# Performance work log

Measured on AMD Instinct MI355X. Metric: run time of the kernel, lower is better.

The kernel has to match this reference:

```python
import jax, jax.numpy as jnp
import numpy as np

B, N, C = 4, 1024, 768          # batch, tokens, embed_dim
D, H, HD, FF = 12, 12, 64, 3072  # depth, heads, head_dim, mlp hidden
LN_EPS = 1e-5


def setup_inputs() -> dict:
    key = jax.random.key(0)
    ks = jax.random.split(key, 12)
    w = lambda i, shape: jax.random.normal(ks[i], shape, jnp.float32) * 0.02
    return {
        "x": jax.random.normal(ks[0], (B, N, C), jnp.float32),
        "pos_x": jax.random.normal(ks[1], (B, N, C), jnp.float32),
        # stacked per-layer params (leading dim D)
        "qkv_w": w(2, (D, 3 * C, C)), "qkv_b": w(3, (D, 3 * C)),
        "proj_w": w(4, (D, C, C)),    "proj_b": w(5, (D, C)),
        "fc1_w": w(6, (D, FF, C)),    "fc1_b": w(7, (D, FF)),
        "fc2_w": w(8, (D, C, FF)),    "fc2_b": w(9, (D, C)),
        "ln1_g": jnp.ones((D, C), jnp.float32), "ln1_b": jnp.zeros((D, C), jnp.float32),
        "ln2_g": jnp.ones((D, C), jnp.float32), "ln2_b": jnp.zeros((D, C), jnp.float32),
        "normf_g": jnp.ones((C,), jnp.float32), "normf_b": jnp.zeros((C,), jnp.float32),
    }


def _ln(x, g, b):
    mu = jnp.mean(x, axis=-1, keepdims=True)
    var = jnp.mean((x - mu) ** 2, axis=-1, keepdims=True)
    return (x - mu) * jax.lax.rsqrt(var + LN_EPS) * g + b


def reference(x, pos_x, qkv_w, qkv_b, proj_w, proj_b, fc1_w, fc1_b, fc2_w, fc2_b,
              ln1_g, ln1_b, ln2_g, ln2_b, normf_g, normf_b):
    scale = 1.0 / jnp.sqrt(jnp.float32(HD))
    x = x + pos_x  # pos added once (add_pos_at_every_layer=False)

    def block(xc, p):
        qw, qb, pw, pb, f1w, f1b, f2w, f2b, g1, b1, g2, b2 = p
        h = _ln(xc, g1, b1)
        qkv = jnp.einsum('bnc,oc->bno', h, qw) + qb            # [B,N,3C]
        qkv = qkv.reshape(B, N, 3, H, HD).transpose(2, 0, 3, 1, 4)
        q, k, v = qkv[0], qkv[1], qkv[2]                       # [B,H,N,HD]
        attn = jax.nn.softmax(jnp.einsum('bhnd,bhmd->bhnm', q, k) * scale, axis=-1)
        o = jnp.einsum('bhnm,bhmd->bhnd', attn, v)
        o = o.transpose(0, 2, 1, 3).reshape(B, N, C)
        xc = xc + (jnp.einsum('bnc,oc->bno', o, pw) + pb)      # residual + proj
        h2 = _ln(xc, g2, b2)
        hid = jax.nn.gelu(jnp.einsum('bnc,fc->bnf', h2, f1w) + f1b, approximate=False)
        ffn = jnp.einsum('bnf,of->bno', hid, f2w) + f2b
        xc = xc + ffn
        return xc, None

    xs = (qkv_w, qkv_b, proj_w, proj_b, fc1_w, fc1_b, fc2_w, fc2_b,
          ln1_g, ln1_b, ln2_g, ln2_b)
    x, _ = jax.lax.scan(block, x, xs)
    return _ln(x, normf_g, normf_b)  # postnorm
```

## Files before the change

kernel.cpp:

```cpp
#include <hip/hip_runtime.h>
#include <hip/hip_bf16.h>
#include <math.h>

typedef __bf16 bf16;
typedef __bf16 bf16x8 __attribute__((ext_vector_type(8)));
typedef __bf16 bf16x4 __attribute__((ext_vector_type(4)));
typedef float  f32x4  __attribute__((ext_vector_type(4)));

#define B_  4
#define N_  1024
#define C_  768
#define H_  12
#define HD_ 64
#define FF_ 3072
#define T_  (B_*N_)
#define D_  12

__device__ __forceinline__ void gld_lds16(const void* g, void* l) {
    __builtin_amdgcn_global_load_lds(
        (const __attribute__((address_space(1))) void*)g,
        (__attribute__((address_space(3))) void*)l, 16, 0, 0);
}

__device__ __forceinline__ float gelu_f(float v) {
    const float ax = fabsf(v) * 0.70710678118f;
    const float t  = __frcp_rn(1.0f + 0.3275911f * ax);
    float p = 1.061405429f;
    p = p * t - 1.453152027f;
    p = p * t + 1.421413741f;
    p = p * t - 0.284496736f;
    p = p * t + 0.254829592f;
    const float e = p * t * __expf(-ax * ax);
    const float erfv = (v >= 0.f) ? (1.0f - e) : (e - 1.0f);
    return 0.5f * v * (1.0f + erfv);
}

template<typename WT, int MODE>
__global__ __launch_bounds__(256) void gemm_bt(
    const bf16* __restrict__ A, const WT* __restrict__ Bt,
    const float* __restrict__ bias, bf16* __restrict__ out,
    float* __restrict__ resid, int M, int N, int Kfull, int Ks)
{
    constexpr int NB = (sizeof(WT) == 2) ? 2 : 1;
    __shared__ __align__(16) bf16 lA[NB][128*64];
    __shared__ __align__(16) WT   lB[NB][128*64];
    const int tid  = threadIdx.x;
    const int lane = tid & 63, wave = tid >> 6;
    const int lo = lane & 15, hi = lane >> 4;
    const int wm = wave & 1, wn = wave >> 1;

    const int nblk = gridDim.x;
    const int id2  = (blockIdx.x & 7) * (nblk >> 3) + (blockIdx.x >> 3);
    const int gx = M >> 7, gy = N >> 7;
    const int bx  = id2 % gx;
    const int byz = id2 / gx;
    const int by  = byz % gy;
    const int bz  = byz / gy;
    const int row0 = bx * 128, col0 = by * 128;
    const int k0base = bz * Ks;
    const int nt = Ks >> 6;

    f32x4 acc[4][4];
#pragma unroll
    for (int i = 0; i < 4; i++)
#pragma unroll
        for (int j = 0; j < 4; j++) acc[i][j] = (f32x4){0.f, 0.f, 0.f, 0.f};

    auto stageA = [&](int t, int buf) {
#pragma unroll
        for (int r = 0; r < 4; ++r) {
            const int cb    = r * 256 + wave * 64;
            const int chunk = cb + lane;
            const int rw = chunk >> 3, kc = chunk & 7;
            const int kcs = kc ^ (rw & 7);
            gld_lds16(A + (size_t)(row0 + rw) * Kfull + k0base + t * 64 + kcs * 8,
                      lA[buf] + cb * 8);
        }
    };
    auto stageB = [&](int t, int buf) {
        if constexpr (sizeof(WT) == 2) {
#pragma unroll
            for (int r = 0; r < 4; ++r) {
                const int cb    = r * 256 + wave * 64;
                const int chunk = cb + lane;
                const int rw = chunk >> 3, kc = chunk & 7;
                const int kcs = kc ^ (rw & 7);
                gld_lds16(Bt + (size_t)(col0 + rw) * Kfull + k0base + t * 64 + kcs * 8,
                          (bf16*)lB[buf] + cb * 8);
            }
        } else {
#pragma unroll
            for (int r = 0; r < 8; ++r) {
                const int cb    = r * 256 + wave * 64;
                const int chunk = cb + lane;
                const int rw = chunk >> 4, kc = chunk & 15;
                const int kcs = kc ^ ((rw & 7) << 1);
                gld_lds16(Bt + (size_t)(col0 + rw) * Kfull + k0base + t * 64 + kcs * 4,
                          (float*)lB[buf] + cb * 4);
            }
        }
    };
    auto compute = [&](int buf) {
#pragma unroll 1
        for (int s = 0; s < 2; ++s) {
            bf16x8 af[4], bfr[4];
#pragma unroll
            for (int i = 0; i < 4; i++) {
                const int rowA = wm * 64 + i * 16 + lo;
                const int ca = (s * 4 + hi) ^ (lo & 7);
                af[i] = *(const bf16x8*)(lA[buf] + rowA * 64 + ca * 8);
            }
#pragma unroll
            for (int i = 0; i < 4; i++) {
                const int rowB = wn * 64 + i * 16 + lo;
                if constexpr (sizeof(WT) == 2) {
                    const int cc = (s * 4 + hi) ^ (lo & 7);
                    bfr[i] = *(const bf16x8*)((const bf16*)lB[buf] + rowB * 64 + cc * 8);
                } else {
                    const float* base = (const float*)lB[buf] + rowB * 64;
                    const int c0 = (s * 8 + hi * 2) ^ ((lo & 7) << 1);
                    const f32x4 u0 = *(const f32x4*)(base + c0 * 4);
                    const f32x4 u1 = *(const f32x4*)(base + (c0 + 1) * 4);
                    bf16x8 f;
#pragma unroll
                    for (int e = 0; e < 4; e++) { f[e] = (bf16)u0[e]; f[4+e] = (bf16)u1[e]; }
                    bfr[i] = f;
                }
            }
#pragma unroll
            for (int mi = 0; mi < 4; mi++)
#pragma unroll
                for (int ni = 0; ni < 4; ni++)
                    acc[mi][ni] = __builtin_amdgcn_mfma_f32_16x16x32_bf16(
                        af[mi], bfr[ni], acc[mi][ni], 0, 0, 0);
        }
    };

    if constexpr (NB == 2) {
        stageA(0, 0); stageB(0, 0);
        __syncthreads();
        int cur = 0;
        for (int t = 0; t < nt; ++t) {
            if (t + 1 < nt) { stageA(t + 1, cur ^ 1); stageB(t + 1, cur ^ 1); }
            compute(cur);
            __syncthreads();
            cur ^= 1;
        }
    } else {
        for (int t = 0; t < nt; ++t) {
            stageA(t, 0); stageB(t, 0);
            __syncthreads();
            compute(0);
            __syncthreads();
        }
    }

    const float bscale = (bz == 0) ? 1.0f : 0.0f;
#pragma unroll
    for (int mi = 0; mi < 4; mi++) {
#pragma unroll
        for (int ni = 0; ni < 4; ni++) {
            const int gcol = col0 + wn * 64 + ni * 16 + lo;
            const float bv = bias[gcol] * bscale;
#pragma unroll
            for (int r = 0; r < 4; r++) {
                const int grow = row0 + wm * 64 + mi * 16 + hi * 4 + r;
                float v = acc[mi][ni][r] + bv;
                if (MODE == 1) v = gelu_f(v);
                if (MODE == 2) {
                    atomicAdd(&resid[(size_t)grow * N + gcol], v);
                } else {
                    out[(size_t)grow * N + gcol] = (bf16)v;
                }
            }
        }
    }
}

__global__ __launch_bounds__(256) void cvt_k(
    const float* __restrict__ src, bf16* __restrict__ dst)
{
    const int i = (blockIdx.x * 256 + threadIdx.x) * 8;
    const f32x4 a = *(const f32x4*)(src + i);
    const f32x4 b = *(const f32x4*)(src + i + 4);
    bf16x8 o;
#pragma unroll
    for (int e = 0; e < 4; e++) { o[e] = (bf16)a[e]; o[4 + e] = (bf16)b[e]; }
    *(bf16x8*)(dst + i) = o;
}

template<typename OutT>
__global__ __launch_bounds__(256) void ln_k(
    const float* __restrict__ x, const float* __restrict__ g,
    const float* __restrict__ b, OutT* __restrict__ out)
{
    const int wave = threadIdx.x >> 6, lane = threadIdx.x & 63;
    const int t = blockIdx.x * 4 + wave;
    const float* row = x + (size_t)t * C_;
    f32x4 v[3];
    float s = 0.f, ss = 0.f;
#pragma unroll
    for (int j = 0; j < 3; j++) {
        v[j] = *(const f32x4*)(row + (j * 64 + lane) * 4);
#pragma unroll
        for (int e = 0; e < 4; e++) { s += v[j][e]; ss += v[j][e] * v[j][e]; }
    }
#pragma unroll
    for (int off = 32; off > 0; off >>= 1) {
        s  += __shfl_xor(s, off);
        ss += __shfl_xor(ss, off);
    }
    const float mu  = s * (1.f / 768.f);
    const float var = ss * (1.f / 768.f) - mu * mu;
    const float rs  = rsqrtf(var + 1e-5f);
    OutT* orow = out + (size_t)t * C_;
#pragma unroll
    for (int j = 0; j < 3; j++) {
        const f32x4 gv = *(const f32x4*)(g + (j * 64 + lane) * 4);
        const f32x4 bv = *(const f32x4*)(b + (j * 64 + lane) * 4);
#pragma unroll
        for (int e = 0; e < 4; e++)
            orow[(j * 64 + lane) * 4 + e] = (OutT)((v[j][e] - mu) * rs * gv[e] + bv[e]);
    }
}

__global__ __launch_bounds__(256) void addpos_k(
    const float* __restrict__ x, const float* __restrict__ p, float* __restrict__ o)
{
    const int i = (blockIdx.x * 256 + threadIdx.x) * 4;
    const f32x4 xv = *(const f32x4*)(x + i);
    const f32x4 pv = *(const f32x4*)(p + i);
    f32x4 ov;
#pragma unroll
    for (int e = 0; e < 4; e++) ov[e] = xv[e] + pv[e];
    *(f32x4*)(o + i) = ov;
}

#define SKD_ 72
#define SVK_ 136
#define SPK_ 136
__global__ __launch_bounds__(256) void attn_k(
    const bf16* __restrict__ qkv, bf16* __restrict__ out)
{
    const int id2 = (blockIdx.x & 7) * 96 + (blockIdx.x >> 3);
    const int qt = id2 & 15;
    const int bh = id2 >> 4;
    const int b = bh / H_, h = bh % H_;
    const int lane = threadIdx.x & 63, wave = threadIdx.x >> 6;
    const int lo = lane & 15, hi = lane >> 4;

    __shared__ __align__(16) bf16 lK[128 * SKD_];
    __shared__ __align__(16) bf16 lV[64 * SVK_];
    __shared__ __align__(16) bf16 lP[4][16 * SPK_];

    const size_t tokbase = (size_t)b * N_;

    const bf16* qptr = qkv + (tokbase + qt * 64 + wave * 16 + lo) * (3 * C_) + h * HD_;
    bf16x8 qf0 = *(const bf16x8*)(qptr + hi * 8);
    bf16x8 qf1 = *(const bf16x8*)(qptr + 32 + hi * 8);
#pragma unroll
    for (int e = 0; e < 8; e++) {
        qf0[e] = (bf16)((float)qf0[e] * 0.125f);
        qf1[e] = (bf16)((float)qf1[e] * 0.125f);
    }

    float m_r[4], l_r[4];
    f32x4 oacc[4];
#pragma unroll
    for (int r = 0; r < 4; r++) { m_r[r] = -1e30f; l_r[r] = 0.f; }
#pragma unroll
    for (int di = 0; di < 4; di++) oacc[di] = (f32x4){0.f, 0.f, 0.f, 0.f};

    for (int kt = 0; kt < 8; ++kt) {
        const int kb0 = kt * 128;
#pragma unroll
        for (int r = 0; r < 4; ++r) {
            const int chunk = r * 256 + threadIdx.x;
            const int key = chunk >> 3, dc = chunk & 7;
            const bf16* kp = qkv + (tokbase + kb0 + key) * (3 * C_) + C_ + h * HD_ + dc * 8;
            *(bf16x8*)(lK + key * SKD_ + dc * 8) = *(const bf16x8*)kp;
        }
#pragma unroll
        for (int r = 0; r < 4; ++r) {
            const int chunk = r * 256 + threadIdx.x;
            const int d = chunk & 63, kg = chunk >> 6;
            const bf16* vp = qkv + (tokbase + kb0 + kg * 8) * (3 * C_)
                           + 2 * C_ + h * HD_ + d;
            bf16x8 tv;
#pragma unroll
            for (int i = 0; i < 8; i++) tv[i] = vp[(size_t)i * (3 * C_)];
            *(bf16x8*)(lV + d * SVK_ + kg * 8) = tv;
        }
        __syncthreads();

        f32x4 sacc[8];
#pragma unroll
        for (int kb = 0; kb < 8; kb++) {
            const bf16x8 b0 = *(const bf16x8*)(lK + (kb * 16 + lo) * SKD_ + hi * 8);
            const bf16x8 b1 = *(const bf16x8*)(lK + (kb * 16 + lo) * SKD_ + 32 + hi * 8);
            f32x4 a = (f32x4){0.f, 0.f, 0.f, 0.f};
            a = __builtin_amdgcn_mfma_f32_16x16x32_bf16(qf0, b0, a, 0, 0, 0);
            a = __builtin_amdgcn_mfma_f32_16x16x32_bf16(qf1, b1, a, 0, 0, 0);
            sacc[kb] = a;
        }

        float pm[4], mn[4], ts[4];
#pragma unroll
        for (int r = 0; r < 4; r++) {
            float a0 = fmaxf(fmaxf(sacc[0][r], sacc[1][r]),
                             fmaxf(sacc[2][r], sacc[3][r]));
            float a1 = fmaxf(fmaxf(sacc[4][r], sacc[5][r]),
                             fmaxf(sacc[6][r], sacc[7][r]));
            pm[r] = fmaxf(a0, a1);
            ts[r] = 0.f;
        }
        const int okd = (pm[0] <= m_r[0] + 8.f) && (pm[1] <= m_r[1] + 8.f)
                     && (pm[2] <= m_r[2] + 8.f) && (pm[3] <= m_r[3] + 8.f);
        const bool defer = __all(okd);
        if (defer) {
#pragma unroll
            for (int r = 0; r < 4; r++) mn[r] = m_r[r];
        } else {
#pragma unroll
            for (int r = 0; r < 4; r++) {
                float tm = pm[r];
#pragma unroll
                for (int off = 1; off < 16; off <<= 1)
                    tm = fmaxf(tm, __shfl_xor(tm, off));
                mn[r] = fmaxf(m_r[r], tm);
            }
        }
#pragma unroll
        for (int kb = 0; kb < 8; kb++)
#pragma unroll
            for (int r = 0; r < 4; r++) {
                const float p = __expf(sacc[kb][r] - mn[r]);
                lP[wave][(hi * 4 + r) * SPK_ + kb * 16 + lo] = (bf16)p;
                ts[r] += p;
            }
#pragma unroll
        for (int r = 0; r < 4; r++)
#pragma unroll
            for (int off = 1; off < 16; off <<= 1)
                ts[r] += __shfl_xor(ts[r], off);
        if (defer) {
#pragma unroll
            for (int r = 0; r < 4; r++) l_r[r] += ts[r];
        } else {
            float alpha[4];
#pragma unroll
            for (int r = 0; r < 4; r++) {
                alpha[r] = __expf(m_r[r] - mn[r]);
                l_r[r] = l_r[r] * alpha[r] + ts[r];
                m_r[r] = mn[r];
            }
#pragma unroll
            for (int di = 0; di < 4; di++)
#pragma unroll
                for (int r = 0; r < 4; r++) oacc[di][r] *= alpha[r];
        }

        bf16x8 pa[4];
#pragma unroll
        for (int s = 0; s < 4; s++)
            pa[s] = *(const bf16x8*)(&lP[wave][lo * SPK_ + s * 32 + hi * 8]);
#pragma unroll
        for (int di = 0; di < 4; di++) {
#pragma unroll
            for (int s = 0; s < 4; s++) {
                const bf16x8 v = *(const bf16x8*)(lV + (di * 16 + lo) * SVK_ + s * 32 + hi * 8);
                oacc[di] = __builtin_amdgcn_mfma_f32_16x16x32_bf16(pa[s], v, oacc[di], 0, 0, 0);
            }
        }
        __syncthreads();
    }

    float il[4];
#pragma unroll
    for (int r = 0; r < 4; r++) il[r] = 1.0f / l_r[r];
#pragma unroll
    for (int di = 0; di < 4; di++)
#pragma unroll
        for (int r = 0; r < 4; r++) {
            const size_t tok = tokbase + qt * 64 + wave * 16 + hi * 4 + r;
            out[tok * C_ + h * HD_ + di * 16 + lo] = (bf16)(oacc[di][r] * il[r]);
        }
}

extern "C" void kernel_launch(void* const* d_in, const int* in_sizes, int n_in,
                              void* d_out, int out_size, void* d_ws, size_t ws_size,
                              hipStream_t stream)
{
    const float* x      = (const float*)d_in[0];
    const float* pos_x  = (const float*)d_in[1];
    const float* qkv_w  = (const float*)d_in[2];
    const float* qkv_b  = (const float*)d_in[3];
    const float* proj_w = (const float*)d_in[4];
    const float* proj_b = (const float*)d_in[5];
    const float* fc1_w  = (const float*)d_in[6];
    const float* fc1_b  = (const float*)d_in[7];
    const float* fc2_w  = (const float*)d_in[8];
    const float* fc2_b  = (const float*)d_in[9];
    const float* ln1_g  = (const float*)d_in[10];
    const float* ln1_b  = (const float*)d_in[11];
    const float* ln2_g  = (const float*)d_in[12];
    const float* ln2_b  = (const float*)d_in[13];
    const float* nf_g   = (const float*)d_in[14];
    const float* nf_b   = (const float*)d_in[15];

    char* ws = (char*)d_ws;
    float* xres  = (float*)(ws);
    bf16* hbuf   = (bf16*)(ws + 12582912);
    bf16* qkvbuf = (bf16*)(ws + 18874368);
    bf16* attno  = (bf16*)(ws + 37748736);
    bf16* hid    = (bf16*)(ws + 44040192);
    bf16* wq     = (bf16*)(ws + 69206016);
    bf16* wp     = (bf16*)(ws + 111673344);
    bf16* w1     = (bf16*)(ws + 125829120);
    bf16* w2     = (bf16*)(ws + 182452224);
    const bool usebf16 = ws_size >= (size_t)239075328;

    addpos_k<<<T_ * C_ / 4 / 256, 256, 0, stream>>>(x, pos_x, xres);

    if (usebf16) {
        cvt_k<<<D_ * 3 * C_ * C_ / 2048, 256, 0, stream>>>(qkv_w, wq);
        cvt_k<<<D_ * C_ * C_ / 2048, 256, 0, stream>>>(proj_w, wp);
        cvt_k<<<D_ * FF_ * C_ / 2048, 256, 0, stream>>>(fc1_w, w1);
        cvt_k<<<D_ * C_ * FF_ / 2048, 256, 0, stream>>>(fc2_w, w2);
    }

    const int g_qkv  = (T_/128) * ((3*C_)/128);
    const int g_proj = (T_/128) * (C_/128) * 2;
    const int g_fc1  = (T_/128) * (FF_/128);
    const int g_fc2  = (T_/128) * (C_/128) * 2;

    for (int L = 0; L < D_; ++L) {
        ln_k<bf16><<<T_ / 4, 256, 0, stream>>>(xres, ln1_g + L * C_, ln1_b + L * C_, hbuf);
        if (usebf16) {
            gemm_bt<bf16,0><<<g_qkv, 256, 0, stream>>>(
                hbuf, wq + (size_t)L * 3 * C_ * C_, qkv_b + (size_t)L * 3 * C_,
                qkvbuf, nullptr, T_, 3 * C_, C_, C_);
        } else {
            gemm_bt<float,0><<<g_qkv, 256, 0, stream>>>(
                hbuf, qkv_w + (size_t)L * 3 * C_ * C_, qkv_b + (size_t)L * 3 * C_,
                qkvbuf, nullptr, T_, 3 * C_, C_, C_);
        }
        attn_k<<<N_ / 64 * B_ * H_, 256, 0, stream>>>(qkvbuf, attno);
        if (usebf16) {
            gemm_bt<bf16,2><<<g_proj, 256, 0, stream>>>(
                attno, wp + (size_t)L * C_ * C_, proj_b + (size_t)L * C_,
                nullptr, xres, T_, C_, C_, C_ / 2);
        } else {
            gemm_bt<float,2><<<g_proj, 256, 0, stream>>>(
                attno, proj_w + (size_t)L * C_ * C_, proj_b + (size_t)L * C_,
                nullptr, xres, T_, C_, C_, C_ / 2);
        }
        ln_k<bf16><<<T_ / 4, 256, 0, stream>>>(xres, ln2_g + L * C_, ln2_b + L * C_, hbuf);
        if (usebf16) {
            gemm_bt<bf16,1><<<g_fc1, 256, 0, stream>>>(
                hbuf, w1 + (size_t)L * FF_ * C_, fc1_b + (size_t)L * FF_,
                hid, nullptr, T_, FF_, C_, C_);
            gemm_bt<bf16,2><<<g_fc2, 256, 0, stream>>>(
                hid, w2 + (size_t)L * C_ * FF_, fc2_b + (size_t)L * C_,
                nullptr, xres, T_, C_, FF_, FF_ / 2);
        } else {
            gemm_bt<float,1><<<g_fc1, 256, 0, stream>>>(
                hbuf, fc1_w + (size_t)L * FF_ * C_, fc1_b + (size_t)L * FF_,
                hid, nullptr, T_, FF_, C_, C_);
            gemm_bt<float,2><<<g_fc2, 256, 0, stream>>>(
                hid, fc2_w + (size_t)L * C_ * FF_, fc2_b + (size_t)L * C_,
                nullptr, xres, T_, C_, FF_, FF_ / 2);
        }
    }
    ln_k<float><<<T_ / 4, 256, 0, stream>>>(xres, nf_g, nf_b, (float*)d_out);
}
```

Measured before the change: 2.878 ms.

## Triple-buffer bf16 GEMM with BK=32 and explicit vmcnt waits

Changes the bf16-weight GEMM path from double-buffered BK=64 tiles to triple-buffered BK=32 tiles. It prefetches two stages ahead and uses explicit s_waitcnt vmcnt counts with raw barriers instead of __syncthreads, so global loads overlap compute more. The LDS footprint per block shrinks, which may raise occupancy, but each barrier now covers only half as much MFMA work. The fp32-weight path is inlined and keeps the same behaviour.

```diff
diff --git a/kernel.cpp b/kernel.cpp
--- a/kernel.cpp
+++ b/kernel.cpp
@@ -21,6 +21,9 @@
         (const __attribute__((address_space(1))) void*)g,
         (__attribute__((address_space(3))) void*)l, 16, 0, 0);
 }
+
+#define WAITV(N) asm volatile("s_waitcnt vmcnt(" #N ")" ::: "memory")
+#define WAITL0() asm volatile("s_waitcnt lgkmcnt(0)" ::: "memory")
 
 __device__ __forceinline__ float gelu_f(float v) {
     const float ax = fabsf(v) * 0.70710678118f;
@@ -41,9 +44,11 @@
     const float* __restrict__ bias, bf16* __restrict__ out,
     float* __restrict__ resid, int M, int N, int Kfull, int Ks)
 {
-    constexpr int NB = (sizeof(WT) == 2) ? 2 : 1;
-    __shared__ __align__(16) bf16 lA[NB][128*64];
-    __shared__ __align__(16) WT   lB[NB][128*64];
+    constexpr bool BF  = (sizeof(WT) == 2);
+    constexpr int  BK  = BF ? 32 : 64;
+    constexpr int  NBF = BF ? 3 : 1;
+    __shared__ __align__(16) bf16 lA[NBF][128*BK];
+    __shared__ __align__(16) WT   lB[NBF][128*BK];
     const int tid  = threadIdx.x;
     const int lane = tid & 63, wave = tid >> 6;
     const int lo = lane & 15, hi = lane >> 4;
@@ -58,7 +63,7 @@
     const int bz  = byz / gy;
     const int row0 = bx * 128, col0 = by * 128;
     const int k0base = bz * Ks;
-    const int nt = Ks >> 6;
+    const int nt = Ks / BK;
 
     f32x4 acc[4][4];
 #pragma unroll
@@ -66,29 +71,84 @@
 #pragma unroll
         for (int j = 0; j < 4; j++) acc[i][j] = (f32x4){0.f, 0.f, 0.f, 0.f};
 
-    auto stageA = [&](int t, int buf) {
-#pragma unroll
-        for (int r = 0; r < 4; ++r) {
-            const int cb    = r * 256 + wave * 64;
-            const int chunk = cb + lane;
-            const int rw = chunk >> 3, kc = chunk & 7;
-            const int kcs = kc ^ (rw & 7);
-            gld_lds16(A + (size_t)(row0 + rw) * Kfull + k0base + t * 64 + kcs * 8,
-                      lA[buf] + cb * 8);
-        }
-    };
-    auto stageB = [&](int t, int buf) {
-        if constexpr (sizeof(WT) == 2) {
+    if constexpr (BF) {
+        auto stageA = [&](int t, int buf) {
+#pragma unroll
+            for (int r = 0; r < 2; ++r) {
+                const int cb    = r * 256 + wave * 64;
+                const int chunk = cb + lane;
+                const int rw = chunk >> 2, kc = chunk & 3;
+                const int kcs = kc ^ (rw & 3);
+                gld_lds16(A + (size_t)(row0 + rw) * Kfull + k0base + t * 32 + kcs * 8,
+                          lA[buf] + cb * 8);
+            }
+        };
+        auto stageB = [&](int t, int buf) {
+#pragma unroll
+            for (int r = 0; r < 2; ++r) {
+                const int cb    = r * 256 + wave * 64;
+                const int chunk = cb + lane;
+                const int rw = chunk >> 2, kc = chunk & 3;
+                const int kcs = kc ^ (rw & 3);
+                gld_lds16(Bt + (size_t)(col0 + rw) * Kfull + k0base + t * 32 + kcs * 8,
+                          (bf16*)lB[buf] + cb * 8);
+            }
+        };
+        auto compute = [&](int buf) {
+            bf16x8 af[4], bfr[4];
+#pragma unroll
+            for (int i = 0; i < 4; i++) {
+                const int rowA = wm * 64 + i * 16 + lo;
+                const int ca = hi ^ (lo & 3);
+                af[i] = *(const bf16x8*)(lA[buf] + rowA * 32 + ca * 8);
+            }
+#pragma unroll
+            for (int i = 0; i < 4; i++) {
+                const int rowB = wn * 64 + i * 16 + lo;
+                const int cc = hi ^ (lo & 3);
+                bfr[i] = *(const bf16x8*)((const bf16*)lB[buf] + rowB * 32 + cc * 8);
+            }
+#pragma unroll
+            for (int mi = 0; mi < 4; mi++)
+#pragma unroll
+                for (int ni = 0; ni < 4; ni++)
+                    acc[mi][ni] = __builtin_amdgcn_mfma_f32_16x16x32_bf16(
+                        af[mi], bfr[ni], acc[mi][ni], 0, 0, 0);
+        };
+
+        stageA(0, 0); stageB(0, 0);
+        stageA(1, 1); stageB(1, 1);
+        int cur = 0;
+#pragma unroll 1
+        for (int t = 0; t < nt; ++t) {
+            if (t + 2 < nt) {
+                const int nx = (cur >= 1) ? cur - 1 : 2;
+                stageA(t + 2, nx); stageB(t + 2, nx);
+                WAITV(8);
+            } else if (t + 1 < nt) {
+                WAITV(4);
+            } else {
+                WAITV(0);
+            }
+            __builtin_amdgcn_s_barrier();
+            __builtin_amdgcn_sched_barrier(0);
+            compute(cur);
+            WAITL0();
+            __builtin_amdgcn_sched_barrier(0);
+            __builtin_amdgcn_s_barrier();
+            cur = (cur == 2) ? 0 : cur + 1;
+        }
+    } else {
+        for (int t = 0; t < nt; ++t) {
 #pragma unroll
             for (int r = 0; r < 4; ++r) {
                 const int cb    = r * 256 + wave * 64;
                 const int chunk = cb + lane;
                 const int rw = chunk >> 3, kc = chunk & 7;
                 const int kcs = kc ^ (rw & 7);
-                gld_lds16(Bt + (size_t)(col0 + rw) * Kfull + k0base + t * 64 + kcs * 8,
-                          (bf16*)lB[buf] + cb * 8);
-            }
-        } else {
+                gld_lds16(A + (size_t)(row0 + rw) * Kfull + k0base + t * 64 + kcs * 8,
+                          lA[0] + cb * 8);
+            }
 #pragma unroll
             for (int r = 0; r < 8; ++r) {
                 const int cb    = r * 256 + wave * 64;
@@ -96,28 +156,22 @@
                 const int rw = chunk >> 4, kc = chunk & 15;
                 const int kcs = kc ^ ((rw & 7) << 1);
                 gld_lds16(Bt + (size_t)(col0 + rw) * Kfull + k0base + t * 64 + kcs * 4,
-                          (float*)lB[buf] + cb * 4);
-            }
-        }
-    };
-    auto compute = [&](int buf) {
+                          (float*)lB[0] + cb * 4);
+            }
+            __syncthreads();
 #pragma unroll 1
-        for (int s = 0; s < 2; ++s) {
-            bf16x8 af[4], bfr[4];
-#pragma unroll
-            for (int i = 0; i < 4; i++) {
-                const int rowA = wm * 64 + i * 16 + lo;
-                const int ca = (s * 4 + hi) ^ (lo & 7);
-                af[i] = *(const bf16x8*)(lA[buf] + rowA * 64 + ca * 8);
-            }
-#pragma unroll
-            for (int i = 0; i < 4; i++) {
-                const int rowB = wn * 64 + i * 16 + lo;
-                if constexpr (sizeof(WT) == 2) {
-                    const int cc = (s * 4 + hi) ^ (lo & 7);
-                    bfr[i] = *(const bf16x8*)((const bf16*)lB[buf] + rowB * 64 + cc * 8);
-                } else {
-                    const float* base = (const float*)lB[buf] + rowB * 64;
+            for (int s = 0; s < 2; ++s) {
+                bf16x8 af[4], bfr[4];
+#pragma unroll
+                for (int i = 0; i < 4; i++) {
+                    const int rowA = wm * 64 + i * 16 + lo;
+                    const int ca = (s * 4 + hi) ^ (lo & 7);
+                    af[i] = *(const bf16x8*)(lA[0] + rowA * 64 + ca * 8);
+                }
+#pragma unroll
+                for (int i = 0; i < 4; i++) {
+                    const int rowB = wn * 64 + i * 16 + lo;
+                    const float* base = (const float*)lB[0] + rowB * 64;
                     const int c0 = (s * 8 + hi * 2) ^ ((lo & 7) << 1);
                     const f32x4 u0 = *(const f32x4*)(base + c0 * 4);
                     const f32x4 u1 = *(const f32x4*)(base + (c0 + 1) * 4);
@@ -126,31 +180,13 @@
                     for (int e = 0; e < 4; e++) { f[e] = (bf16)u0[e]; f[4+e] = (bf16)u1[e]; }
                     bfr[i] = f;
                 }
-            }
-#pragma unroll
-            for (int mi = 0; mi < 4; mi++)
-#pragma unroll
-                for (int ni = 0; ni < 4; ni++)
-                    acc[mi][ni] = __builtin_amdgcn_mfma_f32_16x16x32_bf16(
-                        af[mi], bfr[ni], acc[mi][ni], 0, 0, 0);
-        }
-    };
-
-    if constexpr (NB == 2) {
-        stageA(0, 0); stageB(0, 0);
-        __syncthreads();
-        int cur = 0;
-        for (int t = 0; t < nt; ++t) {
-            if (t + 1 < nt) { stageA(t + 1, cur ^ 1); stageB(t + 1, cur ^ 1); }
-            compute(cur);
-            __syncthreads();
-            cur ^= 1;
-        }
-    } else {
-        for (int t = 0; t < nt; ++t) {
-            stageA(t, 0); stageB(t, 0);
-            __syncthreads();
-            compute(0);
+#pragma unroll
+                for (int mi = 0; mi < 4; mi++)
+#pragma unroll
+                    for (int ni = 0; ni < 4; ni++)
+                        acc[mi][ni] = __builtin_amdgcn_mfma_f32_16x16x32_bf16(
+                            af[mi], bfr[ni], acc[mi][ni], 0, 0, 0);
+            }
             __syncthreads();
         }
     }
```

After: 2.925 ms. No clear change (+1.6%).
